# Performance work log

Measured on AMD Instinct MI355X. Metric: run time of the kernel, lower is better.

Reference implementation:

```python
import jax, jax.numpy as jnp
import numpy as np
import math

N_NODES = 100000
N_EDGES = 1600000
INPUT_SIZE = 256
N_HEADS = 8
HEAD_SIZE = INPUT_SIZE // N_HEADS  # 32
DK = math.sqrt(HEAD_SIZE)


def setup_inputs() -> dict:
    key = jax.random.key(0)
    k1, k2, k3, k4, k5 = jax.random.split(key, 5)
    X = jax.random.normal(k1, (N_NODES, INPUT_SIZE), dtype=jnp.float32)
    edge_index = jax.random.randint(k2, (2, N_EDGES), 0, N_NODES, dtype=jnp.int64)
    # kaiming_normal (fan_in = input_size) std = sqrt(2/fan_in)
    std = math.sqrt(2.0 / INPUT_SIZE)
    Wq = jax.random.normal(k3, (INPUT_SIZE, HEAD_SIZE), dtype=jnp.float32) * std
    Wk = jax.random.normal(k4, (INPUT_SIZE, HEAD_SIZE), dtype=jnp.float32) * std
    Wv = jax.random.normal(k5, (INPUT_SIZE, HEAD_SIZE), dtype=jnp.float32) * std
    return {"X": X, "edge_index": edge_index, "Wq": Wq, "Wk": Wk, "Wv": Wv}


def reference(X, edge_index, Wq, Wk, Wv):
    N = X.shape[0]
    Q = X @ Wq  # [N, h]
    K = X @ Wk  # [N, h]
    V = X @ Wv  # [N, h]
    src = edge_index[0]  # row index (softmax over dim=1 -> per-src segments)
    dst = edge_index[1]
    # per-edge QK dot, scaled
    scores = jnp.sum(Q[src] * K[dst], axis=-1) / DK  # [E]
    # segment-wise (sparse) softmax over each row
    row_max = jax.ops.segment_max(scores, src, num_segments=N)  # [N]
    ex = jnp.exp(scores - row_max[src])  # [E]
    denom = jax.ops.segment_sum(ex, src, num_segments=N)  # [N]
    alpha = ex / denom[src]  # [E]
    # sparse-mm aggregate of V: out[i] = sum_j alpha_ij * V[j]
    out = jax.ops.segment_sum(alpha[:, None] * V[dst], src, num_segments=N)  # [N, h]
    return out
```

## Files before the change

kernel.cpp:

```cpp
#include <hip/hip_runtime.h>

#define N_INPUT 256
#define HS 32

#define BKT_SHIFT 7
#define BKT_NODES 128
#define NBUCK_MAX 800
#define CAP 2560
#define EPB 2048

typedef __attribute__((ext_vector_type(8))) short bf16x8;
typedef __attribute__((ext_vector_type(4))) float f32x4;
typedef __attribute__((ext_vector_type(8))) unsigned short u16x8;

__device__ __forceinline__ unsigned short f2bf(float f) {
    unsigned u = __float_as_uint(f);
    unsigned r = u + 0x7FFFu + ((u >> 16) & 1u);
    return (unsigned short)(r >> 16);
}
__device__ __forceinline__ float bf2f(unsigned short u) {
    return __uint_as_float((unsigned)u << 16);
}

__global__ void zero_gtail_kernel(int* __restrict__ gtail, int nb) {
    int t = threadIdx.x;
    for (int i = t; i < nb; i += 256) gtail[i] = 0;
}

union MegaSmem {
    unsigned short sB[6 * 8 * 64 * 8];
    struct { int h[NBUCK_MAX]; int bs[NBUCK_MAX]; } p;
};

__global__ __launch_bounds__(256) void mega_kernel(
        const float* __restrict__ X, const float* __restrict__ Wq,
        const float* __restrict__ Wk, const float* __restrict__ Wv,
        const int* __restrict__ src, const int* __restrict__ dst,
        float* __restrict__ Q, unsigned short* __restrict__ KVb,
        int* __restrict__ gtail, uint2* __restrict__ staging,
        int N, int E, int nb, int s1blocks) {
    __shared__ MegaSmem u;
    int tid = threadIdx.x;

    if ((int)blockIdx.x < s1blocks) {
        int e0 = blockIdx.x * EPB;
        for (int i = tid; i < nb; i += 256) u.p.h[i] = 0;
        __syncthreads();
        int ss[8], dd[8], rr[8];
#pragma unroll
        for (int k = 0; k < 8; ++k) {
            int i = e0 + tid + k * 256;
            ss[k] = -1;
            if (i < E) {
                int s = src[i];
                dd[k] = dst[i];
                ss[k] = s;
                rr[k] = atomicAdd(&u.p.h[s >> BKT_SHIFT], 1);
            }
        }
        __syncthreads();
        for (int b = tid; b < nb; b += 256) {
            int c = u.p.h[b];
            u.p.bs[b] = c ? atomicAdd(&gtail[b], c) : 0;
        }
        __syncthreads();
#pragma unroll
        for (int k = 0; k < 8; ++k) {
            if (ss[k] >= 0) {
                int b = ss[k] >> BKT_SHIFT;
                int pos = u.p.bs[b] + rr[k];
                if (pos < CAP)
                    staging[(size_t)b * CAP + pos] =
                        make_uint2((unsigned)ss[k], (unsigned)dd[k]);
            }
        }
        return;
    }

    int bq = blockIdx.x - s1blocks;
    for (int i = 0; i < 12; ++i) {
        int c = tid + i * 256;
        int s = c >> 9;
        int t = (c >> 6) & 7;
        int L = c & 63;
        const float* wm = (s < 2) ? Wq : (s < 4) ? Wk : Wv;
        const float* wsrc = wm + (size_t)(t * 32 + (L >> 4) * 8) * HS + (s & 1) * 16 + (L & 15);
        unsigned e0 = f2bf(wsrc[0 * HS]) | ((unsigned)f2bf(wsrc[1 * HS]) << 16);
        unsigned e1 = f2bf(wsrc[2 * HS]) | ((unsigned)f2bf(wsrc[3 * HS]) << 16);
        unsigned e2 = f2bf(wsrc[4 * HS]) | ((unsigned)f2bf(wsrc[5 * HS]) << 16);
        unsigned e3 = f2bf(wsrc[6 * HS]) | ((unsigned)f2bf(wsrc[7 * HS]) << 16);
        ((uint4*)u.sB)[c] = make_uint4(e0, e1, e2, e3);
    }
    __syncthreads();

    int wave = tid >> 6;
    int L = tid & 63;
    int quad = L >> 4;
    int lane16 = L & 15;
    int mt = bq * 4 + wave;
    if (mt * 16 >= N) return;

    const float* xrow = X + (size_t)(mt * 16 + lane16) * N_INPUT + quad * 8;
    bf16x8 afrag[8];
#pragma unroll
    for (int t = 0; t < 8; ++t) {
        float4 a0 = *(const float4*)(xrow + t * 32);
        float4 a1 = *(const float4*)(xrow + t * 32 + 4);
        bf16x8 f;
        f[0] = (short)f2bf(a0.x); f[1] = (short)f2bf(a0.y);
        f[2] = (short)f2bf(a0.z); f[3] = (short)f2bf(a0.w);
        f[4] = (short)f2bf(a1.x); f[5] = (short)f2bf(a1.y);
        f[6] = (short)f2bf(a1.z); f[7] = (short)f2bf(a1.w);
        afrag[t] = f;
    }

#pragma unroll
    for (int s = 0; s < 6; ++s) {
        f32x4 acc = {0.f, 0.f, 0.f, 0.f};
#pragma unroll
        for (int t = 0; t < 8; ++t) {
            bf16x8 bfrag = *((const bf16x8*)u.sB + (s * 8 + t) * 64 + L);
            acc = __builtin_amdgcn_mfma_f32_16x16x32_bf16(afrag[t], bfrag, acc, 0, 0, 0);
        }
        int col = (s & 1) * 16 + lane16;
#pragma unroll
        for (int r = 0; r < 4; ++r) {
            int row = mt * 16 + quad * 4 + r;
            if (s < 2) {
                Q[(size_t)row * HS + col] = acc[r];
            } else {
                size_t pos = (size_t)row * 64 + (size_t)(col >> 2) * 8 +
                             ((s < 4) ? 0 : 4) + (col & 3);
                KVb[pos] = f2bf(acc[r]);
            }
        }
    }
}

__global__ __launch_bounds__(512) void s2_agg_kernel(
        const uint2* __restrict__ staging, const int* __restrict__ gtail,
        const float* __restrict__ Q, const unsigned short* __restrict__ KVb,
        float* __restrict__ out, int N) {
    __shared__ int ldst[CAP];
    __shared__ int nh[BKT_NODES];
    __shared__ int nx[BKT_NODES];
    __shared__ int rk[BKT_NODES];
    int b = blockIdx.x;
    int t = threadIdx.x;
    int cnt = min(gtail[b], CAP);
    if (t < BKT_NODES) { nh[t] = 0; rk[t] = 0; }
    __syncthreads();
    uint2 stash[5];
#pragma unroll
    for (int k = 0; k < 5; ++k) {
        int i = t + k * 512;
        if (i < cnt) {
            uint2 e = staging[(size_t)b * CAP + i];
            stash[k] = e;
            atomicAdd(&nh[e.x & (BKT_NODES - 1)], 1);
        }
    }
    __syncthreads();
    if (t < BKT_NODES) nx[t] = nh[t];
    __syncthreads();
    for (int off = 1; off < BKT_NODES; off <<= 1) {
        int u = (t >= off && t < BKT_NODES) ? nx[t - off] : 0;
        __syncthreads();
        if (t < BKT_NODES) nx[t] += u;
        __syncthreads();
    }
#pragma unroll
    for (int k = 0; k < 5; ++k) {
        int i = t + k * 512;
        if (i < cnt) {
            uint2 e = stash[k];
            int sl = (int)(e.x & (BKT_NODES - 1));
            int r = atomicAdd(&rk[sl], 1);
            ldst[nx[sl] - nh[sl] + r] = (int)e.y;
        }
    }
    __syncthreads();

    int lane = t & 31;
    int grp = t >> 5;
    int slot = lane >> 3;
    int sub = lane & 7;
    int node0 = b << BKT_SHIFT;
    for (int ni = grp; ni < BKT_NODES; ni += 16) {
        int n = node0 + ni;
        if (n >= N) continue;
        int end = nx[ni];
        int beg = end - nh[ni];
        float4 qf = *(const float4*)(Q + (size_t)n * HS + sub * 4);
        float4 acc = make_float4(0.f, 0.f, 0.f, 0.f);
        float den = 0.f;
        for (int j = beg; j < end; j += 4) {
            int e = j + slot;
            bool valid = e < end;
            int d = valid ? ldst[e] : 0;
            u16x8 kv = *(const u16x8*)(KVb + (size_t)d * 64 + sub * 8);
            float p = qf.x * bf2f(kv[0]) + qf.y * bf2f(kv[1]) +
                      qf.z * bf2f(kv[2]) + qf.w * bf2f(kv[3]);
            p += __shfl_xor(p, 1, 32);
            p += __shfl_xor(p, 2, 32);
            p += __shfl_xor(p, 4, 32);
            float ex = valid ? __expf(p * 0.17677669529663687f) : 0.f;
            den += ex;
            acc.x += ex * bf2f(kv[4]);
            acc.y += ex * bf2f(kv[5]);
            acc.z += ex * bf2f(kv[6]);
            acc.w += ex * bf2f(kv[7]);
        }
#pragma unroll
        for (int off = 8; off <= 16; off <<= 1) {
            acc.x += __shfl_xor(acc.x, off, 32);
            acc.y += __shfl_xor(acc.y, off, 32);
            acc.z += __shfl_xor(acc.z, off, 32);
            acc.w += __shfl_xor(acc.w, off, 32);
            den += __shfl_xor(den, off, 32);
        }
        if (lane < 8) {
            float4 o = make_float4(0.f, 0.f, 0.f, 0.f);
            if (end > beg) {
                float rd = 1.f / den;
                o = make_float4(acc.x * rd, acc.y * rd, acc.z * rd, acc.w * rd);
            }
            *(float4*)(out + (size_t)n * HS + lane * 4) = o;
        }
    }
}

extern "C" void kernel_launch(void* const* d_in, const int* in_sizes, int n_in,
                              void* d_out, int out_size, void* d_ws, size_t ws_size,
                              hipStream_t stream) {
    const float* X  = (const float*)d_in[0];
    const int*   ei = (const int*)d_in[1];
    const float* Wq = (const float*)d_in[2];
    const float* Wk = (const float*)d_in[3];
    const float* Wv = (const float*)d_in[4];

    int N = in_sizes[0] / N_INPUT;
    int E = in_sizes[1] / 2;
    const int* src = ei;
    const int* dst = ei + E;

    float* ws = (float*)d_ws;
    float* Q = ws;
    unsigned short* KVb = (unsigned short*)(Q + (size_t)N * HS);
    int* gtail = (int*)(KVb + (size_t)N * 64);
    uint2* staging = (uint2*)(gtail + NBUCK_MAX);
    float* out = (float*)d_out;

    int nbuck = (N + BKT_NODES - 1) >> BKT_SHIFT;
    int s1blocks = (E + EPB - 1) / EPB;
    int mtiles = (N + 15) / 16;
    int qblocks = (mtiles + 3) / 4;

    zero_gtail_kernel<<<1, 256, 0, stream>>>(gtail, nbuck);
    mega_kernel<<<s1blocks + qblocks, 256, 0, stream>>>(
        X, Wq, Wk, Wv, src, dst, Q, KVb, gtail, staging, N, E, nbuck, s1blocks);
    s2_agg_kernel<<<nbuck, 512, 0, stream>>>(staging, gtail, Q, KVb, out, N);
}
```

Baseline: 248.8 us.

## Pre-pack bf16 weights once in prep kernel and interleave scatter/GEMM blocks

Moves the fp32-to-bf16 weight conversion and MFMA-fragment packing out of every projection block into a small prep kernel that writes packed weights to workspace. The projection blocks then read B fragments straight from global memory (L2-cached) instead of building them in shared memory, which removes a per-block prologue and a barrier and lowers LDS use. Block indices are also interleaved so every third block does edge bucketing, mixing the memory-bound scatter work with the MFMA projection work across the GPU. The cost is global/L2 loads for B fragments in the inner loop and somewhat more complex index math.

```diff
diff --git a/kernel.cpp b/kernel.cpp
--- a/kernel.cpp
+++ b/kernel.cpp
@@ -22,29 +22,44 @@
     return __uint_as_float((unsigned)u << 16);
 }
 
-__global__ void zero_gtail_kernel(int* __restrict__ gtail, int nb) {
+__global__ void prep_kernel(int* __restrict__ gtail, int nb,
+                            const float* __restrict__ Wq,
+                            const float* __restrict__ Wk,
+                            const float* __restrict__ Wv,
+                            uint4* __restrict__ Wp) {
     int t = threadIdx.x;
-    for (int i = t; i < nb; i += 256) gtail[i] = 0;
-}
-
-union MegaSmem {
-    unsigned short sB[6 * 8 * 64 * 8];
-    struct { int h[NBUCK_MAX]; int bs[NBUCK_MAX]; } p;
-};
+    if (blockIdx.x == 0) {
+        for (int i = t; i < nb; i += 256) gtail[i] = 0;
+        return;
+    }
+    int c = (int)(blockIdx.x - 1) * 256 + t;
+    int s = c >> 9;
+    int tt = (c >> 6) & 7;
+    int L = c & 63;
+    const float* wm = (s < 2) ? Wq : (s < 4) ? Wk : Wv;
+    const float* wsrc = wm + (size_t)(tt * 32 + (L >> 4) * 8) * HS + (s & 1) * 16 + (L & 15);
+    unsigned e0 = f2bf(wsrc[0 * HS]) | ((unsigned)f2bf(wsrc[1 * HS]) << 16);
+    unsigned e1 = f2bf(wsrc[2 * HS]) | ((unsigned)f2bf(wsrc[3 * HS]) << 16);
+    unsigned e2 = f2bf(wsrc[4 * HS]) | ((unsigned)f2bf(wsrc[5 * HS]) << 16);
+    unsigned e3 = f2bf(wsrc[6 * HS]) | ((unsigned)f2bf(wsrc[7 * HS]) << 16);
+    Wp[c] = make_uint4(e0, e1, e2, e3);
+}
 
 __global__ __launch_bounds__(256) void mega_kernel(
-        const float* __restrict__ X, const float* __restrict__ Wq,
-        const float* __restrict__ Wk, const float* __restrict__ Wv,
+        const float* __restrict__ X, const uint4* __restrict__ Wp,
         const int* __restrict__ src, const int* __restrict__ dst,
         float* __restrict__ Q, unsigned short* __restrict__ KVb,
         int* __restrict__ gtail, uint2* __restrict__ staging,
         int N, int E, int nb, int s1blocks) {
-    __shared__ MegaSmem u;
+    __shared__ int sh[NBUCK_MAX];
+    __shared__ int sbs[NBUCK_MAX];
     int tid = threadIdx.x;
-
-    if ((int)blockIdx.x < s1blocks) {
-        int e0 = blockIdx.x * EPB;
-        for (int i = tid; i < nb; i += 256) u.p.h[i] = 0;
+    int idx = (int)blockIdx.x;
+    bool is_s1 = (idx % 3 == 0) && (idx / 3 < s1blocks);
+
+    if (is_s1) {
+        int e0 = (idx / 3) * EPB;
+        for (int i = tid; i < nb; i += 256) sh[i] = 0;
         __syncthreads();
         int ss[8], dd[8], rr[8];
 #pragma unroll
@@ -55,20 +70,20 @@
                 int s = src[i];
                 dd[k] = dst[i];
                 ss[k] = s;
-                rr[k] = atomicAdd(&u.p.h[s >> BKT_SHIFT], 1);
+                rr[k] = atomicAdd(&sh[s >> BKT_SHIFT], 1);
             }
         }
         __syncthreads();
         for (int b = tid; b < nb; b += 256) {
-            int c = u.p.h[b];
-            u.p.bs[b] = c ? atomicAdd(&gtail[b], c) : 0;
+            int c = sh[b];
+            sbs[b] = c ? atomicAdd(&gtail[b], c) : 0;
         }
         __syncthreads();
 #pragma unroll
         for (int k = 0; k < 8; ++k) {
             if (ss[k] >= 0) {
                 int b = ss[k] >> BKT_SHIFT;
-                int pos = u.p.bs[b] + rr[k];
+                int pos = sbs[b] + rr[k];
                 if (pos < CAP)
                     staging[(size_t)b * CAP + pos] =
                         make_uint2((unsigned)ss[k], (unsigned)dd[k]);
@@ -77,22 +92,7 @@
         return;
     }
 
-    int bq = blockIdx.x - s1blocks;
-    for (int i = 0; i < 12; ++i) {
-        int c = tid + i * 256;
-        int s = c >> 9;
-        int t = (c >> 6) & 7;
-        int L = c & 63;
-        const float* wm = (s < 2) ? Wq : (s < 4) ? Wk : Wv;
-        const float* wsrc = wm + (size_t)(t * 32 + (L >> 4) * 8) * HS + (s & 1) * 16 + (L & 15);
-        unsigned e0 = f2bf(wsrc[0 * HS]) | ((unsigned)f2bf(wsrc[1 * HS]) << 16);
-        unsigned e1 = f2bf(wsrc[2 * HS]) | ((unsigned)f2bf(wsrc[3 * HS]) << 16);
-        unsigned e2 = f2bf(wsrc[4 * HS]) | ((unsigned)f2bf(wsrc[5 * HS]) << 16);
-        unsigned e3 = f2bf(wsrc[6 * HS]) | ((unsigned)f2bf(wsrc[7 * HS]) << 16);
-        ((uint4*)u.sB)[c] = make_uint4(e0, e1, e2, e3);
-    }
-    __syncthreads();
-
+    int bq = idx - min(idx / 3 + 1, s1blocks);
     int wave = tid >> 6;
     int L = tid & 63;
     int quad = L >> 4;
@@ -119,7 +119,7 @@
         f32x4 acc = {0.f, 0.f, 0.f, 0.f};
 #pragma unroll
         for (int t = 0; t < 8; ++t) {
-            bf16x8 bfrag = *((const bf16x8*)u.sB + (s * 8 + t) * 64 + L);
+            bf16x8 bfrag = ((const bf16x8*)Wp)[(s * 8 + t) * 64 + L];
             acc = __builtin_amdgcn_mfma_f32_16x16x32_bf16(afrag[t], bfrag, acc, 0, 0, 0);
         }
         int col = (s & 1) * 16 + lane16;
@@ -247,7 +247,8 @@
     float* ws = (float*)d_ws;
     float* Q = ws;
     unsigned short* KVb = (unsigned short*)(Q + (size_t)N * HS);
-    int* gtail = (int*)(KVb + (size_t)N * 64);
+    uint4* Wp = (uint4*)(KVb + (size_t)N * 64);
+    int* gtail = (int*)(Wp + 3072);
     uint2* staging = (uint2*)(gtail + NBUCK_MAX);
     float* out = (float*)d_out;
 
@@ -256,8 +257,8 @@
     int mtiles = (N + 15) / 16;
     int qblocks = (mtiles + 3) / 4;
 
-    zero_gtail_kernel<<<1, 256, 0, stream>>>(gtail, nbuck);
+    prep_kernel<<<13, 256, 0, stream>>>(gtail, nbuck, Wq, Wk, Wv, Wp);
     mega_kernel<<<s1blocks + qblocks, 256, 0, stream>>>(
-        X, Wq, Wk, Wv, src, dst, Q, KVb, gtail, staging, N, E, nbuck, s1blocks);
+        X, Wp, src, dst, Q, KVb, gtail, staging, N, E, nbuck, s1blocks);
     s2_agg_kernel<<<nbuck, 512, 0, stream>>>(staging, gtail, Q, KVb, out, N);
 }
```

Result: faster. 231.8 us (-6.8%).
